# Optimization experiments

Measured on AMD Instinct MI355X. Metric: run time of the kernel, lower is better.

## Reference

```python
import jax, jax.numpy as jnp
import numpy as np

EPS_NORM = 1e-12  # torch F.normalize eps
EPS_SQRT = 1e-6
EPS_DIV = 1e-6


def setup_inputs() -> dict:
    key = jax.random.key(0)
    k1, k2, k3 = jax.random.split(key, 3)
    B, K, D, C = 4096, 32768, 256, 100
    def l2n(x):
        return x / jnp.maximum(jnp.linalg.norm(x, axis=1, keepdims=True), EPS_NORM)
    batch_feature = l2n(jax.random.normal(k1, (B, D), dtype=jnp.float32))
    queue_emb_copy = l2n(jax.random.normal(k2, (K, D), dtype=jnp.float32))
    info_label = jax.random.randint(k3, (K,), 0, C, dtype=jnp.int64 if jax.config.jax_enable_x64 else jnp.int32)
    return {"batch_feature": batch_feature, "queue_emb_copy": queue_emb_copy,
            "info_label": info_label, "num_classes": C}


def reference(batch_feature, queue_emb_copy, info_label, num_classes):
    # Per-class centroids: segment-mean over the queue (replaces the torch.where loop).
    counts = jax.ops.segment_sum(jnp.ones((queue_emb_copy.shape[0],), queue_emb_copy.dtype),
                                 info_label, num_segments=num_classes)  # [C]
    sums = jax.ops.segment_sum(queue_emb_copy, info_label, num_segments=num_classes)  # [C, D]
    centroids = sums / counts[:, None]
    centroids_norm = centroids / jnp.maximum(jnp.linalg.norm(centroids, axis=1, keepdims=True), EPS_NORM)

    # Pseudo-labels from similarity to centroids.
    similarity_matrix_cls = batch_feature @ centroids_norm.T  # [B, C]
    pseudo_label = jnp.argmax(similarity_matrix_cls, axis=1)  # [B]
    mask = (pseudo_label[:, None] == info_label[None, :])     # [B, K] bool

    # Pairwise MAE distances (unit-norm embeddings: MSE = 2 - 2*cos).
    sim_matrix = jnp.einsum('bc,kc->bk', batch_feature, jax.lax.stop_gradient(queue_emb_copy))
    MAE_matrix = jnp.sqrt(2.0 - 2.0 * sim_matrix + EPS_SQRT)  # [B, K]

    maskf = mask.astype(MAE_matrix.dtype)
    min_entropy_loss = jnp.mean(jnp.sum(MAE_matrix * maskf, axis=1) / (jnp.sum(maskf, axis=1) + EPS_DIV))
    maskc = 1.0 - maskf
    avg_inter_cluster_dist = jnp.mean(jnp.sum(MAE_matrix * maskc, axis=1) / (jnp.sum(maskc, axis=1) + EPS_DIV))
    max_entropy_loss = 2.0 - avg_inter_cluster_dist
    return min_entropy_loss + max_entropy_loss
```

## Files before the change

### kernel.cpp

```cpp
#include <hip/hip_runtime.h>

#define B_ROWS 4096
#define K_Q    32768
#define D_DIM  256
#define C_CLS  100

typedef unsigned char u8;
typedef __attribute__((ext_vector_type(4))) int i32x4;
typedef __attribute__((ext_vector_type(8))) int i32x8;
typedef __attribute__((ext_vector_type(16))) float f32x16;

__device__ inline float fast_sqrt(float x) { return __builtin_amdgcn_sqrtf(x); }

__device__ inline i32x8 mk8(i32x4 lo, i32x4 hi) {
  return __builtin_shufflevector(lo, hi, 0, 1, 2, 3, 4, 5, 6, 7);
}

#define GLDS16(g, l) __builtin_amdgcn_global_load_lds( \
    (const __attribute__((address_space(1))) unsigned int*)(g), \
    (__attribute__((address_space(3))) unsigned int*)(l), 16, 0, 0)


__global__ __launch_bounds__(512) void k_hist(
    const float* __restrict__ q, const int* __restrict__ lab,
    float* __restrict__ partial, u8* __restrict__ qf8,
    float* __restrict__ S_all, float* __restrict__ S_match) {
  __shared__ float lsum[C_CLS * 64];
  const int kc = blockIdx.x, dc = blockIdx.y;
  const int tid = threadIdx.x, w = tid >> 6, l = tid & 63;
  if (dc == 0 && tid < 64) {
    S_all[kc * 64 + tid] = 0.f;
    S_match[kc * 64 + tid] = 0.f;
  }
  for (int i = tid; i < C_CLS * 64; i += 512) lsum[i] = 0.f;
  __syncthreads();
  const int col = dc * 64 + l;
  const int k0 = kc * 512 + w * 64;
  #pragma unroll 4
  for (int r = 0; r < 64; ++r) {
    const int k = k0 + r;
    const int c = lab[k];
    float v = q[(size_t)k * D_DIM + col];
    atomicAdd(&lsum[c * 64 + l], v);
    int p8 = __builtin_amdgcn_cvt_pk_fp8_f32(v * 16.f, v * 16.f, 0, false);
    qf8[(size_t)k * D_DIM + col] = (u8)p8;
  }
  __syncthreads();
  float* pb = partial + (size_t)(kc * 4 + dc) * (C_CLS * 64);
  for (int i = tid; i < C_CLS * 64; i += 512) pb[i] = lsum[i];
}

__global__ __launch_bounds__(256) void k_cnorm(
    const int* __restrict__ lab, const float* __restrict__ partial,
    int* __restrict__ counts, float* __restrict__ cnorm) {
  __shared__ float red[4];
  __shared__ int credi[4];
  const int c = blockIdx.x, d = threadIdx.x;
  int cnt = 0;
  #pragma unroll 8
  for (int i = 0; i < K_Q / 256; ++i) cnt += (lab[d + i * 256] == c) ? 1 : 0;
  #pragma unroll
  for (int o = 1; o < 64; o <<= 1) cnt += __shfl_xor(cnt, o);
  if ((d & 63) == 0) credi[d >> 6] = cnt;
  float s = 0.f;
  const int dcsel = d >> 6, low = d & 63;
  for (int kc = 0; kc < 64; ++kc)
    s += partial[(size_t)(kc * 4 + dcsel) * (C_CLS * 64) + c * 64 + low];
  __syncthreads();
  const int cnt_all = credi[0] + credi[1] + credi[2] + credi[3];
  float v = s / (float)cnt_all;
  float ss = v * v;
  #pragma unroll
  for (int o = 1; o < 64; o <<= 1) ss += __shfl_xor(ss, o);
  if ((d & 63) == 0) red[d >> 6] = ss;
  __syncthreads();
  float norm = sqrtf(red[0] + red[1] + red[2] + red[3]);
  cnorm[c * D_DIM + d] = v / fmaxf(norm, 1e-12f);
  if (d == 0) counts[c] = cnt_all;
}

__global__ void k_pseudo(const float* __restrict__ bf, const float* __restrict__ cn,
                         int* __restrict__ pseudo, u8* __restrict__ af8) {
  const int tid = threadIdx.x;
  const int rloc = tid >> 4, sub = tid & 15;
  const int row = blockIdx.x * 16 + rloc;
  float4 a[4];
  const float4* ap = (const float4*)(bf + (size_t)row * D_DIM);
  #pragma unroll
  for (int j = 0; j < 4; ++j) a[j] = ap[sub + j * 16];
  #pragma unroll
  for (int j = 0; j < 4; ++j) {
    int lo = __builtin_amdgcn_cvt_pk_fp8_f32(a[j].x * 16.f, a[j].y * 16.f, 0, false);
    int pk = __builtin_amdgcn_cvt_pk_fp8_f32(a[j].z * 16.f, a[j].w * 16.f, lo, true);
    *(unsigned int*)(af8 + (size_t)row * D_DIM + (sub + j * 16) * 4) = (unsigned int)pk;
  }
  float best = -1e30f; int bi = 0;
  for (int c = 0; c < C_CLS; c += 2) {
    const float4* cp0 = (const float4*)(cn + c * D_DIM);
    const float4* cp1 = (const float4*)(cn + (c + 1) * D_DIM);
    float s0 = 0.f, s1 = 0.f;
    #pragma unroll
    for (int j = 0; j < 4; ++j) {
      float4 b0 = cp0[sub + j * 16];
      float4 b1 = cp1[sub + j * 16];
      s0 += a[j].x * b0.x + a[j].y * b0.y + a[j].z * b0.z + a[j].w * b0.w;
      s1 += a[j].x * b1.x + a[j].y * b1.y + a[j].z * b1.z + a[j].w * b1.w;
    }
    s0 += __shfl_xor(s0, 1); s1 += __shfl_xor(s1, 1);
    s0 += __shfl_xor(s0, 2); s1 += __shfl_xor(s1, 2);
    s0 += __shfl_xor(s0, 4); s1 += __shfl_xor(s1, 4);
    s0 += __shfl_xor(s0, 8); s1 += __shfl_xor(s1, 8);
    if (s0 > best) { best = s0; bi = c; }
    if (s1 > best) { best = s1; bi = c + 1; }
  }
  if (sub == 0) pseudo[row] = bi;
}

__global__ __launch_bounds__(256, 3) void k_main(
    const u8* __restrict__ Af8, const u8* __restrict__ Qf8,
    const int* __restrict__ lab, const int* __restrict__ pseudo,
    float* __restrict__ S_all, float* __restrict__ S_match) {
  __shared__ u8 Bs[2][64 * 256];

  const int bid = blockIdx.x;
  const int xcd = bid & 7, idx = bid >> 3;
  const int cs = xcd * 4 + (idx >> 5);
  const int rb = idx & 31;

  const int tid = threadIdx.x;
  const int w = tid >> 6, l = tid & 63;
  const int c32 = l & 31, hi32 = l >> 5;
  const int rowA = rb * 128 + w * 32;
  const int colbase = cs * 1024;

  i32x4 areg[4][2];
  {
    const u8* ap = Af8 + (size_t)(rowA + c32) * D_DIM + hi32 * 32;
    #pragma unroll
    for (int ks = 0; ks < 4; ++ks) {
      areg[ks][0] = *(const i32x4*)(ap + ks * 64);
      areg[ks][1] = *(const i32x4*)(ap + ks * 64 + 16);
    }
  }

  int psepk[4];
  #pragma unroll
  for (int g = 0; g < 4; ++g) {
    const int* pp = pseudo + rowA + hi32 * 4 + g * 8;
    psepk[g] = pp[0] | (pp[1] << 8) | (pp[2] << 16) | (pp[3] << 24);
  }

  float pa[16], pm[16];
  #pragma unroll
  for (int r = 0; r < 16; ++r) { pa[r] = 0.f; pm[r] = 0.f; }

  const int strow = tid >> 4;
  const int sinner = (((tid & 15) ^ strow) << 4);
  const u8* sbase = Qf8 + (size_t)(colbase + strow) * D_DIM + sinner;

#define STAGE(buf, ph)                                                    \
  { const u8* s_ = sbase + (size_t)(ph) * (64 * D_DIM);                   \
    _Pragma("unroll")                                                     \
    for (int i_ = 0; i_ < 4; ++i_)                                        \
      GLDS16(s_ + (size_t)i_ * (16 * D_DIM), (buf) + i_ * 4096 + tid * 16); }

  const int* lptr = lab + colbase + c32;
  const int xorm = (c32 & 15) << 4;
  const unsigned int SC1 = 0x7F7F7F7Fu;

  STAGE(&Bs[0][0], 0);

  #pragma unroll 1
  for (int ph = 0; ph < 16; ++ph) {
    __syncthreads();
    if (ph + 1 < 16) STAGE(&Bs[(ph + 1) & 1][0], ph + 1);
    const u8* bs = &Bs[ph & 1][0];
    const int lbl0 = lptr[ph * 64];
    const int lbl1 = lptr[ph * 64 + 32];

    f32x16 acc0{}, acc1{};
    #pragma unroll
    for (int ks = 0; ks < 4; ++ks) {
      const int off = ks * 64 + hi32 * 32;
      i32x4 b0l = *(const i32x4*)(bs + c32 * 256 + (off ^ xorm));
      i32x4 b0h = *(const i32x4*)(bs + c32 * 256 + ((off + 16) ^ xorm));
      i32x4 b1l = *(const i32x4*)(bs + (32 + c32) * 256 + (off ^ xorm));
      i32x4 b1h = *(const i32x4*)(bs + (32 + c32) * 256 + ((off + 16) ^ xorm));
      i32x8 av = mk8(areg[ks][0], areg[ks][1]);
      acc0 = __builtin_amdgcn_mfma_scale_f32_32x32x64_f8f6f4(
          av, mk8(b0l, b0h), acc0, 0, 0, 0, SC1, 0, SC1);
      acc1 = __builtin_amdgcn_mfma_scale_f32_32x32x64_f8f6f4(
          av, mk8(b1l, b1h), acc1, 0, 0, 0, SC1, 0, SC1);
    }

    #pragma unroll
    for (int r = 0; r < 16; ++r) {
      const int p = (psepk[r >> 2] >> ((r & 3) * 8)) & 255;
      float mae0 = fast_sqrt(fmaxf(__builtin_fmaf(-0.0078125f, acc0[r], 2.000001f), 0.0f));
      float mae1 = fast_sqrt(fmaxf(__builtin_fmaf(-0.0078125f, acc1[r], 2.000001f), 0.0f));
      pa[r] += mae0 + mae1;
      pm[r] += (lbl0 == p ? mae0 : 0.0f) + (lbl1 == p ? mae1 : 0.0f);
    }
  }

  #pragma unroll
  for (int r = 0; r < 16; ++r) {
    float va = pa[r], vm = pm[r];
    va += __shfl_xor(va, 1); vm += __shfl_xor(vm, 1);
    va += __shfl_xor(va, 2); vm += __shfl_xor(vm, 2);
    va += __shfl_xor(va, 4); vm += __shfl_xor(vm, 4);
    va += __shfl_xor(va, 8); vm += __shfl_xor(vm, 8);
    va += __shfl_xor(va, 16); vm += __shfl_xor(vm, 16);
    if (c32 == 0) {
      const int gr = rowA + (r & 3) + 8 * (r >> 2) + 4 * hi32;
      atomicAdd(&S_all[gr], va);
      atomicAdd(&S_match[gr], vm);
    }
  }
#undef STAGE
}

__global__ void k_final(const float* __restrict__ S_all, const float* __restrict__ S_match,
                        const int* __restrict__ pseudo, const int* __restrict__ counts,
                        float* __restrict__ out) {
  __shared__ float r1[16], r2[16];
  const int tid = threadIdx.x;
  float s1 = 0.f, s2 = 0.f;
  for (int b = tid; b < B_ROWS; b += 1024) {
    float cnt = (float)counts[pseudo[b]];
    float sm = S_match[b], sa = S_all[b];
    s1 += sm / (cnt + 1e-6f);
    s2 += (sa - sm) / ((float)K_Q - cnt + 1e-6f);
  }
  #pragma unroll
  for (int o = 1; o < 64; o <<= 1) { s1 += __shfl_xor(s1, o); s2 += __shfl_xor(s2, o); }
  if ((tid & 63) == 0) { r1[tid >> 6] = s1; r2[tid >> 6] = s2; }
  __syncthreads();
  if (tid == 0) {
    float t1 = 0.f, t2 = 0.f;
    #pragma unroll
    for (int i = 0; i < 16; ++i) { t1 += r1[i]; t2 += r2[i]; }
    out[0] = t1 / (float)B_ROWS + 2.0f - t2 / (float)B_ROWS;
  }
}

extern "C" void kernel_launch(void* const* d_in, const int* in_sizes, int n_in,
                              void* d_out, int out_size, void* d_ws, size_t ws_size,
                              hipStream_t stream) {
  const float* batch = (const float*)d_in[0];
  const float* queue = (const float*)d_in[1];
  const int*   lab   = (const int*)d_in[2];

  char* ws = (char*)d_ws;
  float* S_all   = (float*)(ws + 0);
  float* S_match = (float*)(ws + 16384);
  int*   counts  = (int*)  (ws + 32768);
  float* cnorm   = (float*)(ws + 33280);
  int*   pseudo  = (int*)  (ws + 135680);
  u8*    Af8     = (u8*)   (ws + 152064);
  u8*    Qf8     = (u8*)   (ws + 1200640);
  float* partial = (float*)(ws + 9589248);

  k_hist  <<<dim3(64, 4), 512, 0, stream>>>(queue, lab, partial, Qf8, S_all, S_match);
  k_cnorm <<<C_CLS, 256, 0, stream>>>(lab, partial, counts, cnorm);
  k_pseudo<<<B_ROWS / 16, 256, 0, stream>>>(batch, cnorm, pseudo, Af8);
  k_main  <<<1024, 256, 0, stream>>>(Af8, Qf8, lab, pseudo, S_all, S_match);
  k_final <<<1, 1024, 0, stream>>>(S_all, S_match, pseudo, counts, (float*)d_out);
}
```

Measured before the change: 151.5 us.

## Fuse final reduction into main kernel via last-block pattern; vectorize histogram loads

Removes the separate k_final launch. The last block of k_main to finish, detected with an atomic done counter, computes the loss reduction instead. k_hist now reads float4 per thread and packs four fp8 values into a single 32-bit store, in place of scalar loads and byte stores, but the shared-memory atomics become scattered across more rows. This adds a threadfence and a global atomic per block to k_main, plus extra layout shifts in the workspace.

```diff
diff --git a/kernel.cpp b/kernel.cpp
--- a/kernel.cpp
+++ b/kernel.cpp
@@ -24,26 +24,35 @@
 __global__ __launch_bounds__(512) void k_hist(
     const float* __restrict__ q, const int* __restrict__ lab,
     float* __restrict__ partial, u8* __restrict__ qf8,
-    float* __restrict__ S_all, float* __restrict__ S_match) {
+    float* __restrict__ S_all, float* __restrict__ S_match,
+    unsigned int* __restrict__ done) {
   __shared__ float lsum[C_CLS * 64];
   const int kc = blockIdx.x, dc = blockIdx.y;
-  const int tid = threadIdx.x, w = tid >> 6, l = tid & 63;
+  const int tid = threadIdx.x;
   if (dc == 0 && tid < 64) {
     S_all[kc * 64 + tid] = 0.f;
     S_match[kc * 64 + tid] = 0.f;
   }
+  if (kc == 0 && dc == 0 && tid == 0) *done = 0u;
   for (int i = tid; i < C_CLS * 64; i += 512) lsum[i] = 0.f;
   __syncthreads();
-  const int col = dc * 64 + l;
-  const int k0 = kc * 512 + w * 64;
+
+  const int rloc = tid >> 4;
+  const int c4 = tid & 15;
   #pragma unroll 4
-  for (int r = 0; r < 64; ++r) {
-    const int k = k0 + r;
+  for (int it = 0; it < 16; ++it) {
+    const int k = kc * 512 + it * 32 + rloc;
     const int c = lab[k];
-    float v = q[(size_t)k * D_DIM + col];
-    atomicAdd(&lsum[c * 64 + l], v);
-    int p8 = __builtin_amdgcn_cvt_pk_fp8_f32(v * 16.f, v * 16.f, 0, false);
-    qf8[(size_t)k * D_DIM + col] = (u8)p8;
+    const size_t off = (size_t)k * D_DIM + dc * 64 + c4 * 4;
+    float4 v = *(const float4*)(q + off);
+    int lo = __builtin_amdgcn_cvt_pk_fp8_f32(v.x * 16.f, v.y * 16.f, 0, false);
+    int pk = __builtin_amdgcn_cvt_pk_fp8_f32(v.z * 16.f, v.w * 16.f, lo, true);
+    *(unsigned int*)(qf8 + off) = (unsigned int)pk;
+    const int base = c * 64 + c4 * 4;
+    atomicAdd(&lsum[base + 0], v.x);
+    atomicAdd(&lsum[base + 1], v.y);
+    atomicAdd(&lsum[base + 2], v.z);
+    atomicAdd(&lsum[base + 3], v.w);
   }
   __syncthreads();
   float* pb = partial + (size_t)(kc * 4 + dc) * (C_CLS * 64);
@@ -119,7 +128,9 @@
 __global__ __launch_bounds__(256, 3) void k_main(
     const u8* __restrict__ Af8, const u8* __restrict__ Qf8,
     const int* __restrict__ lab, const int* __restrict__ pseudo,
-    float* __restrict__ S_all, float* __restrict__ S_match) {
+    float* __restrict__ S_all, float* __restrict__ S_match,
+    const int* __restrict__ counts, unsigned int* __restrict__ done,
+    float* __restrict__ out) {
   __shared__ u8 Bs[2][64 * 256];
 
   const int bid = blockIdx.x;
@@ -218,29 +229,31 @@
     }
   }
 #undef STAGE
-}
-
-__global__ void k_final(const float* __restrict__ S_all, const float* __restrict__ S_match,
-                        const int* __restrict__ pseudo, const int* __restrict__ counts,
-                        float* __restrict__ out) {
-  __shared__ float r1[16], r2[16];
-  const int tid = threadIdx.x;
-  float s1 = 0.f, s2 = 0.f;
-  for (int b = tid; b < B_ROWS; b += 1024) {
-    float cnt = (float)counts[pseudo[b]];
-    float sm = S_match[b], sa = S_all[b];
-    s1 += sm / (cnt + 1e-6f);
-    s2 += (sa - sm) / ((float)K_Q - cnt + 1e-6f);
-  }
-  #pragma unroll
-  for (int o = 1; o < 64; o <<= 1) { s1 += __shfl_xor(s1, o); s2 += __shfl_xor(s2, o); }
-  if ((tid & 63) == 0) { r1[tid >> 6] = s1; r2[tid >> 6] = s2; }
-  __syncthreads();
-  if (tid == 0) {
-    float t1 = 0.f, t2 = 0.f;
-    #pragma unroll
-    for (int i = 0; i < 16; ++i) { t1 += r1[i]; t2 += r2[i]; }
-    out[0] = t1 / (float)B_ROWS + 2.0f - t2 / (float)B_ROWS;
+
+  __threadfence();
+  __shared__ unsigned int isLast;
+  if (tid == 0) isLast = (atomicAdd(done, 1u) == (unsigned)(gridDim.x - 1)) ? 1u : 0u;
+  __syncthreads();
+  if (isLast) {
+    __threadfence();
+    float s1 = 0.f, s2 = 0.f;
+    for (int b = tid; b < B_ROWS; b += 256) {
+      float sa = __hip_atomic_load(&S_all[b], __ATOMIC_RELAXED, __HIP_MEMORY_SCOPE_AGENT);
+      float sm = __hip_atomic_load(&S_match[b], __ATOMIC_RELAXED, __HIP_MEMORY_SCOPE_AGENT);
+      float cnt = (float)counts[pseudo[b]];
+      s1 += sm / (cnt + 1e-6f);
+      s2 += (sa - sm) / ((float)K_Q - cnt + 1e-6f);
+    }
+    #pragma unroll
+    for (int o = 1; o < 64; o <<= 1) { s1 += __shfl_xor(s1, o); s2 += __shfl_xor(s2, o); }
+    __shared__ float r1[4], r2[4];
+    if ((tid & 63) == 0) { r1[tid >> 6] = s1; r2[tid >> 6] = s2; }
+    __syncthreads();
+    if (tid == 0) {
+      float t1 = r1[0] + r1[1] + r1[2] + r1[3];
+      float t2 = r2[0] + r2[1] + r2[2] + r2[3];
+      out[0] = t1 / (float)B_ROWS + 2.0f - t2 / (float)B_ROWS;
+    }
   }
 }
 
@@ -255,15 +268,15 @@
   float* S_all   = (float*)(ws + 0);
   float* S_match = (float*)(ws + 16384);
   int*   counts  = (int*)  (ws + 32768);
-  float* cnorm   = (float*)(ws + 33280);
-  int*   pseudo  = (int*)  (ws + 135680);
-  u8*    Af8     = (u8*)   (ws + 152064);
-  u8*    Qf8     = (u8*)   (ws + 1200640);
-  float* partial = (float*)(ws + 9589248);
-
-  k_hist  <<<dim3(64, 4), 512, 0, stream>>>(queue, lab, partial, Qf8, S_all, S_match);
+  unsigned int* done = (unsigned int*)(ws + 33280);
+  float* cnorm   = (float*)(ws + 33792);
+  int*   pseudo  = (int*)  (ws + 136192);
+  u8*    Af8     = (u8*)   (ws + 152576);
+  u8*    Qf8     = (u8*)   (ws + 1201152);
+  float* partial = (float*)(ws + 9589760);
+
+  k_hist  <<<dim3(64, 4), 512, 0, stream>>>(queue, lab, partial, Qf8, S_all, S_match, done);
   k_cnorm <<<C_CLS, 256, 0, stream>>>(lab, partial, counts, cnorm);
   k_pseudo<<<B_ROWS / 16, 256, 0, stream>>>(batch, cnorm, pseudo, Af8);
-  k_main  <<<1024, 256, 0, stream>>>(Af8, Qf8, lab, pseudo, S_all, S_match);
-  k_final <<<1, 1024, 0, stream>>>(S_all, S_match, pseudo, counts, (float*)d_out);
-}
+  k_main  <<<1024, 256, 0, stream>>>(Af8, Qf8, lab, pseudo, S_all, S_match, counts, done, (float*)d_out);
+}
```

Result: slower. 217.6 us (+43.7%).
